# Performance work log

Measured on AMD Instinct MI355X. Metric: run time of the kernel, lower is better.

## Reference

```python
import jax, jax.numpy as jnp
import numpy as np

N = 50000
E = 400000
D = 128            # embedding_dim
NUM_RBF = 20
CUT_OFF = 5.0
SILU_SCALE = 1.0 / 0.6


def scaled_silu(x):
    return jax.nn.silu(x) * SILU_SCALE


def cosine_cutoff(x):
    return 0.5 * (1.0 + jnp.cos(x * jnp.pi / CUT_OFF)) * (x < CUT_OFF).astype(x.dtype)


def setup_inputs() -> dict:
    key = jax.random.key(0)
    ks = jax.random.split(key, 10)
    vectorial_feat = jax.random.normal(ks[0], (N, D, 3), dtype=jnp.float32)
    scalar_feat = jax.random.normal(ks[1], (N, D), dtype=jnp.float32)
    node_pos = jax.random.uniform(ks[2], (N, 3), dtype=jnp.float32) * 10.0
    source = jax.random.randint(ks[3], (E,), 0, N)
    offset = jax.random.randint(ks[4], (E,), 1, N)  # avoid self-loops -> no zero distance
    target = (source + offset) % N
    edge_index = jnp.stack([source, target], axis=0).astype(jnp.int64)
    # scalar_feat_proj: Linear(D,D) -> ScaledSiLU -> Linear(D, 3D)
    W1 = jax.random.normal(ks[5], (D, D), dtype=jnp.float32) * (1.0 / np.sqrt(D))
    b1 = jnp.zeros((D,), dtype=jnp.float32)
    W2 = jax.random.normal(ks[6], (D, 3 * D), dtype=jnp.float32) * (1.0 / np.sqrt(D))
    b2 = jnp.zeros((3 * D,), dtype=jnp.float32)
    # rbf_proj: Linear(NUM_RBF, 3D)
    Wr = jax.random.normal(ks[7], (NUM_RBF, 3 * D), dtype=jnp.float32) * (1.0 / np.sqrt(NUM_RBF))
    br = jnp.zeros((3 * D,), dtype=jnp.float32)
    return {"vectorial_feat": vectorial_feat, "scalar_feat": scalar_feat,
            "node_pos": node_pos, "edge_index": edge_index,
            "W1": W1, "b1": b1, "W2": W2, "b2": b2, "Wr": Wr, "br": br}


def reference(vectorial_feat, scalar_feat, node_pos, edge_index, W1, b1, W2, b2, Wr, br):
    freqs = jnp.arange(1, NUM_RBF + 1, dtype=jnp.float32) * jnp.pi  # [NUM_RBF]
    source, target = edge_index[0], edge_index[1]

    # node-level scalar projection: [N, 3D]
    s = scaled_silu(scalar_feat @ W1 + b1) @ W2 + b2

    # per-edge geometry
    rel = node_pos[target] - node_pos[source]                 # [E, 3]
    dist = jnp.sqrt(jnp.sum(rel * rel, axis=-1))              # [E]
    dist_scaled = dist / CUT_OFF
    rbf = jnp.sin(freqs[None, :] * dist_scaled[:, None]) / dist[:, None]  # [E, NUM_RBF]

    filt = cosine_cutoff(rbf @ Wr + br)                       # [E, 3D]

    message = (s[source] * filt).reshape(E, D, 3)             # [E, D, 3]
    scalar_msg = message[..., 0]                              # [E, D]
    equiv_msg = message[..., 1]                               # [E, D]
    invar_msg = message[..., 2]                               # [E, D]

    scalar_message = jax.ops.segment_sum(scalar_msg, target, num_segments=N)  # [N, D]

    direction = rel / dist[:, None]                           # [E, 3]
    vec_msg = (invar_msg[:, :, None] * direction[:, None, :]
               + equiv_msg[:, :, None] * vectorial_feat[source])  # [E, D, 3]
    vectorial_message = jax.ops.segment_sum(vec_msg, target, num_segments=N)  # [N, D, 3]

    return vectorial_message, scalar_message
```

## Files before the change

kernel.cpp:

```cpp
#include <hip/hip_runtime.h>
#include <hip/hip_fp16.h>
#include <math.h>
#include <stddef.h>

#define D_DIM 128
#define NUM_RBF 20
typedef unsigned short ushort_t;
typedef unsigned int uint_t;
typedef _Float16 h2v __attribute__((ext_vector_type(2)));
typedef _Float16 half8_t __attribute__((ext_vector_type(8)));
typedef float float4_t __attribute__((ext_vector_type(4)));
constexpr float PI_F = 3.14159265358979323846f;
constexpr float CUT_OFF_F = 5.0f;
constexpr float SILU_SCALE_F = 1.0f / 0.6f;

__device__ __forceinline__ uint_t pack2h(float a, float b) {
  __half2 h2 = __floats2half2_rn(a, b);
  return *reinterpret_cast<uint_t*>(&h2);
}
__device__ __forceinline__ float h2f(ushort_t u) {
  __half h = __ushort_as_half(u);
  return __half2float(h);
}
__device__ __forceinline__ h2v u2h2(uint_t u) {
  h2v r;
  __builtin_memcpy(&r, &u, 4);
  return r;
}

#if defined(__has_builtin)
#if __has_builtin(__builtin_amdgcn_fdot2)
#define HAVE_FDOT2 1
#endif
#endif

__device__ __forceinline__ float fdot2f(h2v a, h2v b, float c) {
#ifdef HAVE_FDOT2
  return __builtin_amdgcn_fdot2(a, b, c, false);
#else
  return c + (float)a.x * (float)b.x + (float)a.y * (float)b.y;
#endif
}

__device__ __forceinline__ void stage_wt(const float* __restrict__ W,
                                         _Float16* __restrict__ Wt, int t,
                                         int f4stride, int f4base) {
  const float4* Wv = reinterpret_cast<const float4*>(W);
#pragma unroll
  for (int i = 0; i < 8; ++i) {
    int pid = t + i * 256;
    int k = (pid >> 5) * 2;
    int nf = pid & 31;
    float4 a = Wv[(size_t)k * f4stride + f4base + nf];
    float4 b = Wv[(size_t)(k + 1) * f4stride + f4base + nf];
    const float av[4] = {a.x, a.y, a.z, a.w};
    const float bv[4] = {b.x, b.y, b.z, b.w};
    const int n0 = nf * 4;
#pragma unroll
    for (int j = 0; j < 4; ++j)
      *reinterpret_cast<uint_t*>(&Wt[(n0 + j) * 136 + k]) =
          pack2h(av[j], bv[j]);
  }
}

__global__ __launch_bounds__(256) void proj_kernel(
    const float* __restrict__ X, const float* __restrict__ W1,
    const float* __restrict__ b1, const float* __restrict__ W2,
    const float* __restrict__ b2, ushort_t* __restrict__ s_half, int N) {
  __shared__ alignas(16) _Float16 Xs[64 * 136];
  __shared__ alignas(16) _Float16 Wt[128 * 136];

  const int t = threadIdx.x;
  const int w = t >> 6;
  const int l = t & 63;
  const int nb = blockIdx.x * 64;

  {
    const float4* Xv = reinterpret_cast<const float4*>(X);
#pragma unroll
    for (int i = 0; i < 8; ++i) {
      int g = t + i * 256;
      int row = g >> 5, k0 = (g & 31) * 4;
      int node = nb + row;
      float4 v = (node < N) ? Xv[(size_t)nb * 32 + g]
                            : make_float4(0.f, 0.f, 0.f, 0.f);
      uint_t* dst = reinterpret_cast<uint_t*>(&Xs[row * 136 + k0]);
      dst[0] = pack2h(v.x, v.y);
      dst[1] = pack2h(v.z, v.w);
    }
  }
  stage_wt(W1, Wt, t, 32, 0);
  __syncthreads();

  const int arow = w * 16 + (l & 15);
  const int koff = (l >> 4) * 8;
  const int bcol = l & 15;

  half8_t af[4];
#pragma unroll
  for (int s = 0; s < 4; ++s)
    af[s] = *reinterpret_cast<const half8_t*>(&Xs[arow * 136 + s * 32 + koff]);

  float4_t acc[8];
#pragma unroll
  for (int c = 0; c < 8; ++c) {
    float4_t a = {0.f, 0.f, 0.f, 0.f};
#pragma unroll
    for (int s = 0; s < 4; ++s) {
      half8_t bf = *reinterpret_cast<const half8_t*>(
          &Wt[(c * 16 + bcol) * 136 + s * 32 + koff]);
      a = __builtin_amdgcn_mfma_f32_16x16x32_f16(af[s], bf, a, 0, 0, 0);
    }
    acc[c] = a;
  }

  __syncthreads();

#pragma unroll
  for (int c = 0; c < 8; ++c) {
    const int col = c * 16 + bcol;
    const float bv = b1[col];
#pragma unroll
    for (int r = 0; r < 4; ++r) {
      const int row = w * 16 + (l >> 4) * 4 + r;
      float hv = acc[c][r] + bv;
      hv = hv * SILU_SCALE_F / (1.0f + expf(-hv));
      Xs[row * 136 + col] = (_Float16)hv;
    }
  }
  stage_wt(W2, Wt, t, 96, 0);
  __syncthreads();

  half8_t ha[4];
#pragma unroll
  for (int s = 0; s < 4; ++s)
    ha[s] = *reinterpret_cast<const half8_t*>(&Xs[arow * 136 + s * 32 + koff]);

  for (int cn = 0; cn < 3; ++cn) {
    if (cn > 0) {
      __syncthreads();
      stage_wt(W2, Wt, t, 96, cn * 32);
      __syncthreads();
    }
#pragma unroll
    for (int c = 0; c < 8; ++c) {
      float4_t a = {0.f, 0.f, 0.f, 0.f};
#pragma unroll
      for (int s = 0; s < 4; ++s) {
        half8_t bf = *reinterpret_cast<const half8_t*>(
            &Wt[(c * 16 + bcol) * 136 + s * 32 + koff]);
        a = __builtin_amdgcn_mfma_f32_16x16x32_f16(ha[s], bf, a, 0, 0, 0);
      }
      const int gcol = cn * 128 + c * 16 + bcol;
      const float bv = b2[gcol];
#pragma unroll
      for (int r = 0; r < 4; ++r) {
        const int node = nb + w * 16 + (l >> 4) * 4 + r;
        if (node < N)
          s_half[(size_t)node * 384 + gcol] =
              __half_as_ushort(__float2half_rn(a[r] + bv));
      }
    }
  }
}

__global__ void vf_cast_kernel(const float* __restrict__ vf,
                               ushort_t* __restrict__ vf_half, int total8) {
  int i = blockIdx.x * 256 + threadIdx.x;
  if (i >= total8) return;
  const float4* v4 = reinterpret_cast<const float4*>(vf);
  float4 a = v4[2 * i], b = v4[2 * i + 1];
  uint4 r = make_uint4(pack2h(a.x, a.y), pack2h(a.z, a.w),
                       pack2h(b.x, b.y), pack2h(b.z, b.w));
  reinterpret_cast<uint4*>(vf_half)[i] = r;
}

__global__ void zero_kernel(int* __restrict__ p, int n) {
  int i = blockIdx.x * 256 + threadIdx.x;
  if (i < n) p[i] = 0;
}

__global__ void hist_kernel(const int* __restrict__ tgt, int* __restrict__ counts,
                            int E) {
  int e = blockIdx.x * 256 + threadIdx.x;
  if (e < E) atomicAdd(&counts[tgt[e]], 1);
}

__global__ void chunk_sum_kernel(const int* __restrict__ counts,
                                 int* __restrict__ chunk_sums, int N) {
  __shared__ int red[256];
  int b = blockIdx.x, t = threadIdx.x;
  int base = b * 1024 + t * 4;
  int s = 0;
#pragma unroll
  for (int j = 0; j < 4; ++j) s += (base + j < N) ? counts[base + j] : 0;
  red[t] = s;
  __syncthreads();
  for (int off = 128; off > 0; off >>= 1) {
    if (t < off) red[t] += red[t + off];
    __syncthreads();
  }
  if (t == 0) chunk_sums[b] = red[0];
}

__global__ void scan_chunks_kernel(int* __restrict__ chunk_sums,
                                   int* __restrict__ offsets, int nch, int N,
                                   int E) {
  int t = threadIdx.x;
  int v = (t < nch) ? chunk_sums[t] : 0;
  int orig = v;
#pragma unroll
  for (int off = 1; off < 64; off <<= 1) {
    int y = __shfl_up(v, off);
    if (t >= off) v += y;
  }
  if (t < nch) chunk_sums[t] = v - orig;
  if (t == 0) offsets[N] = E;
}

__global__ void scan_block_kernel(const int* __restrict__ counts,
                                  const int* __restrict__ chunk_off,
                                  int* __restrict__ offsets,
                                  int* __restrict__ cursor, int N) {
  __shared__ int part[256];
  int b = blockIdx.x, t = threadIdx.x;
  int base = b * 1024 + t * 4;
  int v[4];
#pragma unroll
  for (int j = 0; j < 4; ++j) v[j] = (base + j < N) ? counts[base + j] : 0;
  int local = v[0] + v[1] + v[2] + v[3];
  part[t] = local;
  __syncthreads();
  for (int off = 1; off < 256; off <<= 1) {
    int x = 0;
    if (t >= off) x = part[t - off];
    __syncthreads();
    if (t >= off) part[t] += x;
    __syncthreads();
  }
  int run = chunk_off[b] + (part[t] - local);
#pragma unroll
  for (int j = 0; j < 4; ++j) {
    if (base + j < N) {
      offsets[base + j] = run;
      cursor[base + j] = run;
      run += v[j];
    }
  }
}

__global__ void edge_geom_kernel(const float* __restrict__ pos,
                                 const int* __restrict__ src,
                                 const int* __restrict__ tgt,
                                 int* __restrict__ cursor,
                                 float4* __restrict__ dir4_s,
                                 uint_t* __restrict__ rbh_s,
                                 int* __restrict__ src_s, int E) {
  int e = blockIdx.x * 256 + threadIdx.x;
  if (e >= E) return;
  const int sn = src[e];
  const int tn = tgt[e];
  const float rx = pos[tn * 3 + 0] - pos[sn * 3 + 0];
  const float ry = pos[tn * 3 + 1] - pos[sn * 3 + 1];
  const float rz = pos[tn * 3 + 2] - pos[sn * 3 + 2];
  const float dist = sqrtf(rx * rx + ry * ry + rz * rz);
  const float inv = 1.0f / dist;

  const float ang = dist * (PI_F / CUT_OFF_F);
  float s1, c1;
  sincosf(ang, &s1, &c1);
  float sk = s1, ck = c1;
  float rb[NUM_RBF];
  rb[0] = s1 * inv;
#pragma unroll
  for (int r = 1; r < NUM_RBF; ++r) {
    float sn2 = sk * c1 + ck * s1;
    ck = ck * c1 - sk * s1;
    sk = sn2;
    rb[r] = sk * inv;
  }

  const int p = atomicAdd(&cursor[tn], 1);
  dir4_s[p] = make_float4(rx * inv, ry * inv, rz * inv, dist);
  src_s[p] = sn;
  uint_t us[10];
#pragma unroll
  for (int q = 0; q < 10; ++q) us[q] = pack2h(rb[2 * q], rb[2 * q + 1]);
  uint_t* o = rbh_s + (size_t)p * 12;
  *reinterpret_cast<uint4*>(o) = make_uint4(us[0], us[1], us[2], us[3]);
  *reinterpret_cast<uint4*>(o + 4) = make_uint4(us[4], us[5], us[6], us[7]);
  *reinterpret_cast<uint2*>(o + 8) = make_uint2(us[8], us[9]);
}

#define NODES_PER_BLOCK 16

__device__ __forceinline__ float cutoff_f(float x) {
  return (x < CUT_OFF_F) ? 0.5f * (1.0f + __cosf(x * (PI_F / CUT_OFF_F))) : 0.f;
}

struct EdgeData {
  float4 dir;
  uint_t rbu[10];
  float sx, sy, sz, vx, vy, vz;
};

__device__ __forceinline__ void load_edge(int idx, int sn, int d,
                                          const ushort_t* __restrict__ s_half,
                                          const ushort_t* __restrict__ vf_half,
                                          const float4* __restrict__ dir4_s,
                                          const uint_t* __restrict__ rbh_s,
                                          EdgeData& ed) {
  ed.dir = dir4_s[idx];
  const uint_t* o = rbh_s + (size_t)idx * 12;
  uint4 u0 = *reinterpret_cast<const uint4*>(o);
  uint4 u1 = *reinterpret_cast<const uint4*>(o + 4);
  uint2 u2 = *reinterpret_cast<const uint2*>(o + 8);
  ed.rbu[0] = u0.x; ed.rbu[1] = u0.y; ed.rbu[2] = u0.z; ed.rbu[3] = u0.w;
  ed.rbu[4] = u1.x; ed.rbu[5] = u1.y; ed.rbu[6] = u1.z; ed.rbu[7] = u1.w;
  ed.rbu[8] = u2.x; ed.rbu[9] = u2.y;
  const ushort_t* sr = s_half + (size_t)sn * 384 + 3 * d;
  ed.sx = h2f(sr[0]); ed.sy = h2f(sr[1]); ed.sz = h2f(sr[2]);
  const ushort_t* vr = vf_half + (size_t)sn * 384 + 3 * d;
  ed.vx = h2f(vr[0]); ed.vy = h2f(vr[1]); ed.vz = h2f(vr[2]);
}

__global__ __launch_bounds__(128) void node_kernel(
    const ushort_t* __restrict__ s_half, const ushort_t* __restrict__ vf_half,
    const float4* __restrict__ dir4_s, const uint_t* __restrict__ rbh_s,
    const int* __restrict__ src_s, const int* __restrict__ offsets,
    const float* __restrict__ Wr, const float* __restrict__ br,
    float* __restrict__ out, int N, int E) {
  const int d = threadIdx.x;
  const int lane = d & 63;

  h2v wr0h[10], wr1h[10], wr2h[10];
#pragma unroll
  for (int q = 0; q < 10; ++q) {
    h2v w;
    w.x = (_Float16)Wr[(2 * q) * 384 + 3 * d + 0];
    w.y = (_Float16)Wr[(2 * q + 1) * 384 + 3 * d + 0];
    wr0h[q] = w;
    w.x = (_Float16)Wr[(2 * q) * 384 + 3 * d + 1];
    w.y = (_Float16)Wr[(2 * q + 1) * 384 + 3 * d + 1];
    wr1h[q] = w;
    w.x = (_Float16)Wr[(2 * q) * 384 + 3 * d + 2];
    w.y = (_Float16)Wr[(2 * q + 1) * 384 + 3 * d + 2];
    wr2h[q] = w;
  }
  const float br0 = br[3 * d + 0];
  const float br1 = br[3 * d + 1];
  const float br2 = br[3 * d + 2];

  for (int nn = 0; nn < NODES_PER_BLOCK; ++nn) {
    const int n = blockIdx.x * NODES_PER_BLOCK + nn;
    if (n >= N) break;

    const int start = offsets[n];
    const int end = offsets[n + 1];

    float accs = 0.f, av0 = 0.f, av1 = 0.f, av2 = 0.f;

    for (int base = start; base < end; base += 64) {
      const int m = min(64, end - base);
      int ld = base + lane;
      if (ld >= E) ld = E - 1;
      const int sn_l = src_s[ld];

      int i = 0;
      for (; i + 2 <= m; i += 2) {
        const int sn0 = __shfl(sn_l, i);
        const int sn1 = __shfl(sn_l, i + 1);
        EdgeData e0, e1;
        load_edge(base + i, sn0, d, s_half, vf_half, dir4_s, rbh_s, e0);
        load_edge(base + i + 1, sn1, d, s_half, vf_half, dir4_s, rbh_s, e1);

#pragma unroll
        for (int u = 0; u < 2; ++u) {
          const EdgeData& ed = (u == 0) ? e0 : e1;
          float f0 = br0, f1 = br1, f2 = br2;
#pragma unroll
          for (int q = 0; q < 10; ++q) {
            h2v r = u2h2(ed.rbu[q]);
            f0 = fdot2f(r, wr0h[q], f0);
            f1 = fdot2f(r, wr1h[q], f1);
            f2 = fdot2f(r, wr2h[q], f2);
          }
          f0 = cutoff_f(f0);
          f1 = cutoff_f(f1);
          f2 = cutoff_f(f2);
          const float m0 = ed.sx * f0;
          const float m1 = ed.sy * f1;
          const float m2 = ed.sz * f2;
          accs += m0;
          av0 += m2 * ed.dir.x + m1 * ed.vx;
          av1 += m2 * ed.dir.y + m1 * ed.vy;
          av2 += m2 * ed.dir.z + m1 * ed.vz;
        }
      }
      if (i < m) {
        const int sn0 = __shfl(sn_l, i);
        EdgeData e0;
        load_edge(base + i, sn0, d, s_half, vf_half, dir4_s, rbh_s, e0);
        float f0 = br0, f1 = br1, f2 = br2;
#pragma unroll
        for (int q = 0; q < 10; ++q) {
          h2v r = u2h2(e0.rbu[q]);
          f0 = fdot2f(r, wr0h[q], f0);
          f1 = fdot2f(r, wr1h[q], f1);
          f2 = fdot2f(r, wr2h[q], f2);
        }
        f0 = cutoff_f(f0);
        f1 = cutoff_f(f1);
        f2 = cutoff_f(f2);
        const float m0 = e0.sx * f0;
        const float m1 = e0.sy * f1;
        const float m2 = e0.sz * f2;
        accs += m0;
        av0 += m2 * e0.dir.x + m1 * e0.vx;
        av1 += m2 * e0.dir.y + m1 * e0.vy;
        av2 += m2 * e0.dir.z + m1 * e0.vz;
      }
    }

    out[(size_t)n * 384 + 3 * d + 0] = av0;
    out[(size_t)n * 384 + 3 * d + 1] = av1;
    out[(size_t)n * 384 + 3 * d + 2] = av2;
    out[(size_t)N * 384 + (size_t)n * 128 + d] = accs;
  }
}

extern "C" void kernel_launch(void* const* d_in, const int* in_sizes, int n_in,
                              void* d_out, int out_size, void* d_ws,
                              size_t ws_size, hipStream_t stream) {
  const float* vf  = (const float*)d_in[0];
  const float* X   = (const float*)d_in[1];
  const float* pos = (const float*)d_in[2];
  const int* ei    = (const int*)d_in[3];
  const float* W1  = (const float*)d_in[4];
  const float* b1  = (const float*)d_in[5];
  const float* W2  = (const float*)d_in[6];
  const float* b2  = (const float*)d_in[7];
  const float* Wr  = (const float*)d_in[8];
  const float* br  = (const float*)d_in[9];

  const int N = in_sizes[1] / D_DIM;
  const int E = in_sizes[3] / 2;
  const int* srcI = ei;
  const int* tgtI = ei + E;
  float* out = (float*)d_out;

  char* w = (char*)d_ws;
  float4* dir4_s    = (float4*)w;   w += (size_t)E * sizeof(float4);
  uint_t* rbh_s     = (uint_t*)w;   w += (size_t)E * 12 * sizeof(uint_t);
  ushort_t* s_half  = (ushort_t*)w; w += (size_t)N * 384 * sizeof(ushort_t);
  ushort_t* vf_half = (ushort_t*)w; w += (size_t)N * 384 * sizeof(ushort_t);
  int* src_s        = (int*)w;      w += (size_t)E * sizeof(int);
  int* counts       = (int*)w;      w += (size_t)N * sizeof(int);
  int* offsets      = (int*)w;      w += (size_t)(N + 1) * sizeof(int);
  int* cursor       = (int*)w;      w += (size_t)N * sizeof(int);
  int* chunks       = (int*)w;      w += 64 * sizeof(int);

  const int nch = (N + 1023) / 1024;

  zero_kernel<<<(N + 255) / 256, 256, 0, stream>>>(counts, N);
  proj_kernel<<<(N + 63) / 64, 256, 0, stream>>>(X, W1, b1, W2, b2, s_half, N);
  vf_cast_kernel<<<(N * 384 / 8 + 255) / 256, 256, 0, stream>>>(vf, vf_half,
                                                                N * 384 / 8);
  hist_kernel<<<(E + 255) / 256, 256, 0, stream>>>(tgtI, counts, E);
  chunk_sum_kernel<<<nch, 256, 0, stream>>>(counts, chunks, N);
  scan_chunks_kernel<<<1, 64, 0, stream>>>(chunks, offsets, nch, N, E);
  scan_block_kernel<<<nch, 256, 0, stream>>>(counts, chunks, offsets, cursor, N);
  edge_geom_kernel<<<(E + 255) / 256, 256, 0, stream>>>(pos, srcI, tgtI, cursor,
                                                        dir4_s, rbh_s, src_s, E);
  node_kernel<<<(N + NODES_PER_BLOCK - 1) / NODES_PER_BLOCK, 128, 0, stream>>>(
      s_half, vf_half, dir4_s, rbh_s, src_s, offsets, Wr, br, out, N, E);
}
```

Measured before the change: 311.7 us.

## Fuse vf cast into projection kernel and interleave s and vf per channel

Result: no change. 307.1 us (-1.5%).

```diff
diff --git a/kernel.cpp b/kernel.cpp
--- a/kernel.cpp
+++ b/kernel.cpp
@@ -22,6 +22,8 @@
   __half h = __ushort_as_half(u);
   return __half2float(h);
 }
+__device__ __forceinline__ float h2f_lo(uint_t u) { return h2f((ushort_t)(u & 0xffffu)); }
+__device__ __forceinline__ float h2f_hi(uint_t u) { return h2f((ushort_t)(u >> 16)); }
 __device__ __forceinline__ h2v u2h2(uint_t u) {
   h2v r;
   __builtin_memcpy(&r, &u, 4);
@@ -66,9 +68,11 @@
 __global__ __launch_bounds__(256) void proj_kernel(
     const float* __restrict__ X, const float* __restrict__ W1,
     const float* __restrict__ b1, const float* __restrict__ W2,
-    const float* __restrict__ b2, ushort_t* __restrict__ s_half, int N) {
-  __shared__ alignas(16) _Float16 Xs[64 * 136];
-  __shared__ alignas(16) _Float16 Wt[128 * 136];
+    const float* __restrict__ b2, const float* __restrict__ vf,
+    uint_t* __restrict__ merged, int N) {
+  __shared__ alignas(16) _Float16 smem[26112];
+  _Float16* Xs = smem;
+  _Float16* Wt = smem + 8704;
 
   const int t = threadIdx.x;
   const int w = t >> 6;
@@ -136,6 +140,8 @@
   for (int s = 0; s < 4; ++s)
     ha[s] = *reinterpret_cast<const half8_t*>(&Xs[arow * 136 + s * 32 + koff]);
 
+  uint_t pk[3][8][2];
+#pragma unroll
   for (int cn = 0; cn < 3; ++cn) {
     if (cn > 0) {
       __syncthreads();
@@ -151,28 +157,45 @@
             &Wt[(c * 16 + bcol) * 136 + s * 32 + koff]);
         a = __builtin_amdgcn_mfma_f32_16x16x32_f16(ha[s], bf, a, 0, 0, 0);
       }
-      const int gcol = cn * 128 + c * 16 + bcol;
-      const float bv = b2[gcol];
-#pragma unroll
-      for (int r = 0; r < 4; ++r) {
-        const int node = nb + w * 16 + (l >> 4) * 4 + r;
-        if (node < N)
-          s_half[(size_t)node * 384 + gcol] =
-              __half_as_ushort(__float2half_rn(a[r] + bv));
+      const float bv = b2[cn * 128 + c * 16 + bcol];
+      pk[cn][c][0] = pack2h(a[0] + bv, a[1] + bv);
+      pk[cn][c][1] = pack2h(a[2] + bv, a[3] + bv);
+    }
+  }
+
+  __syncthreads();
+  ushort_t* sh = reinterpret_cast<ushort_t*>(smem);
+  {
+    const int rbase = w * 16 + (l >> 4) * 4;
+#pragma unroll
+    for (int cn = 0; cn < 3; ++cn)
+#pragma unroll
+      for (int c = 0; c < 8; ++c) {
+        const int gcol = cn * 128 + c * 16 + bcol;
+        sh[(rbase + 0) * 392 + gcol] = (ushort_t)(pk[cn][c][0] & 0xffffu);
+        sh[(rbase + 1) * 392 + gcol] = (ushort_t)(pk[cn][c][0] >> 16);
+        sh[(rbase + 2) * 392 + gcol] = (ushort_t)(pk[cn][c][1] & 0xffffu);
+        sh[(rbase + 3) * 392 + gcol] = (ushort_t)(pk[cn][c][1] >> 16);
       }
-    }
-  }
-}
-
-__global__ void vf_cast_kernel(const float* __restrict__ vf,
-                               ushort_t* __restrict__ vf_half, int total8) {
-  int i = blockIdx.x * 256 + threadIdx.x;
-  if (i >= total8) return;
-  const float4* v4 = reinterpret_cast<const float4*>(vf);
-  float4 a = v4[2 * i], b = v4[2 * i + 1];
-  uint4 r = make_uint4(pack2h(a.x, a.y), pack2h(a.z, a.w),
-                       pack2h(b.x, b.y), pack2h(b.z, b.w));
-  reinterpret_cast<uint4*>(vf_half)[i] = r;
+  }
+  __syncthreads();
+
+#pragma unroll 4
+  for (int k = 0; k < 32; ++k) {
+    const int P = k * 256 + t;
+    const int ln = P >> 7;
+    const int chan = P & 127;
+    const int node = nb + ln;
+    if (node < N) {
+      const ushort_t* sp = &sh[ln * 392 + 3 * chan];
+      const float* vp = vf + ((size_t)node * 128 + chan) * 3;
+      uint_t* mp = merged + ((size_t)node * 128 + chan) * 3;
+      mp[0] = (uint_t)sp[0] | ((uint_t)sp[1] << 16);
+      mp[1] = (uint_t)sp[2] |
+              ((uint_t)__half_as_ushort(__float2half_rn(vp[0])) << 16);
+      mp[2] = pack2h(vp[1], vp[2]);
+    }
+  }
 }
 
 __global__ void zero_kernel(int* __restrict__ p, int n) {
@@ -292,7 +315,7 @@
   *reinterpret_cast<uint2*>(o + 8) = make_uint2(us[8], us[9]);
 }
 
-#define NODES_PER_BLOCK 16
+#define NODES_PER_BLOCK 8
 
 __device__ __forceinline__ float cutoff_f(float x) {
   return (x < CUT_OFF_F) ? 0.5f * (1.0f + __cosf(x * (PI_F / CUT_OFF_F))) : 0.f;
@@ -301,12 +324,11 @@
 struct EdgeData {
   float4 dir;
   uint_t rbu[10];
-  float sx, sy, sz, vx, vy, vz;
+  uint_t su[3];
 };
 
 __device__ __forceinline__ void load_edge(int idx, int sn, int d,
-                                          const ushort_t* __restrict__ s_half,
-                                          const ushort_t* __restrict__ vf_half,
+                                          const uint_t* __restrict__ merged,
                                           const float4* __restrict__ dir4_s,
                                           const uint_t* __restrict__ rbh_s,
                                           EdgeData& ed) {
@@ -318,18 +340,15 @@
   ed.rbu[0] = u0.x; ed.rbu[1] = u0.y; ed.rbu[2] = u0.z; ed.rbu[3] = u0.w;
   ed.rbu[4] = u1.x; ed.rbu[5] = u1.y; ed.rbu[6] = u1.z; ed.rbu[7] = u1.w;
   ed.rbu[8] = u2.x; ed.rbu[9] = u2.y;
-  const ushort_t* sr = s_half + (size_t)sn * 384 + 3 * d;
-  ed.sx = h2f(sr[0]); ed.sy = h2f(sr[1]); ed.sz = h2f(sr[2]);
-  const ushort_t* vr = vf_half + (size_t)sn * 384 + 3 * d;
-  ed.vx = h2f(vr[0]); ed.vy = h2f(vr[1]); ed.vz = h2f(vr[2]);
+  const uint_t* mp = merged + ((size_t)sn * 128 + d) * 3;
+  ed.su[0] = mp[0]; ed.su[1] = mp[1]; ed.su[2] = mp[2];
 }
 
 __global__ __launch_bounds__(128) void node_kernel(
-    const ushort_t* __restrict__ s_half, const ushort_t* __restrict__ vf_half,
-    const float4* __restrict__ dir4_s, const uint_t* __restrict__ rbh_s,
-    const int* __restrict__ src_s, const int* __restrict__ offsets,
-    const float* __restrict__ Wr, const float* __restrict__ br,
-    float* __restrict__ out, int N, int E) {
+    const uint_t* __restrict__ merged, const float4* __restrict__ dir4_s,
+    const uint_t* __restrict__ rbh_s, const int* __restrict__ src_s,
+    const int* __restrict__ offsets, const float* __restrict__ Wr,
+    const float* __restrict__ br, float* __restrict__ out, int N, int E) {
   const int d = threadIdx.x;
   const int lane = d & 63;
 
@@ -371,8 +390,8 @@
         const int sn0 = __shfl(sn_l, i);
         const int sn1 = __shfl(sn_l, i + 1);
         EdgeData e0, e1;
-        load_edge(base + i, sn0, d, s_half, vf_half, dir4_s, rbh_s, e0);
-        load_edge(base + i + 1, sn1, d, s_half, vf_half, dir4_s, rbh_s, e1);
+        load_edge(base + i, sn0, d, merged, dir4_s, rbh_s, e0);
+        load_edge(base + i + 1, sn1, d, merged, dir4_s, rbh_s, e1);
 
 #pragma unroll
         for (int u = 0; u < 2; ++u) {
@@ -388,19 +407,19 @@
           f0 = cutoff_f(f0);
           f1 = cutoff_f(f1);
           f2 = cutoff_f(f2);
-          const float m0 = ed.sx * f0;
-          const float m1 = ed.sy * f1;
-          const float m2 = ed.sz * f2;
+          const float m0 = h2f_lo(ed.su[0]) * f0;
+          const float m1 = h2f_hi(ed.su[0]) * f1;
+          const float m2 = h2f_lo(ed.su[1]) * f2;
           accs += m0;
-          av0 += m2 * ed.dir.x + m1 * ed.vx;
-          av1 += m2 * ed.dir.y + m1 * ed.vy;
-          av2 += m2 * ed.dir.z + m1 * ed.vz;
+          av0 += m2 * ed.dir.x + m1 * h2f_hi(ed.su[1]);
+          av1 += m2 * ed.dir.y + m1 * h2f_lo(ed.su[2]);
+          av2 += m2 * ed.dir.z + m1 * h2f_hi(ed.su[2]);
         }
       }
       if (i < m) {
         const int sn0 = __shfl(sn_l, i);
         EdgeData e0;
-        load_edge(base + i, sn0, d, s_half, vf_half, dir4_s, rbh_s, e0);
+        load_edge(base + i, sn0, d, merged, dir4_s, rbh_s, e0);
         float f0 = br0, f1 = br1, f2 = br2;
 #pragma unroll
         for (int q = 0; q < 10; ++q) {
@@ -412,13 +431,13 @@
         f0 = cutoff_f(f0);
         f1 = cutoff_f(f1);
         f2 = cutoff_f(f2);
-        const float m0 = e0.sx * f0;
-        const float m1 = e0.sy * f1;
-        const float m2 = e0.sz * f2;
+        const float m0 = h2f_lo(e0.su[0]) * f0;
+        const float m1 = h2f_hi(e0.su[0]) * f1;
+        const float m2 = h2f_lo(e0.su[1]) * f2;
         accs += m0;
-        av0 += m2 * e0.dir.x + m1 * e0.vx;
-        av1 += m2 * e0.dir.y + m1 * e0.vy;
-        av2 += m2 * e0.dir.z + m1 * e0.vz;
+        av0 += m2 * e0.dir.x + m1 * h2f_hi(e0.su[1]);
+        av1 += m2 * e0.dir.y + m1 * h2f_lo(e0.su[2]);
+        av2 += m2 * e0.dir.z + m1 * h2f_hi(e0.su[2]);
       }
     }
 
@@ -450,22 +469,20 @@
   float* out = (float*)d_out;
 
   char* w = (char*)d_ws;
-  float4* dir4_s    = (float4*)w;   w += (size_t)E * sizeof(float4);
-  uint_t* rbh_s     = (uint_t*)w;   w += (size_t)E * 12 * sizeof(uint_t);
-  ushort_t* s_half  = (ushort_t*)w; w += (size_t)N * 384 * sizeof(ushort_t);
-  ushort_t* vf_half = (ushort_t*)w; w += (size_t)N * 384 * sizeof(ushort_t);
-  int* src_s        = (int*)w;      w += (size_t)E * sizeof(int);
-  int* counts       = (int*)w;      w += (size_t)N * sizeof(int);
-  int* offsets      = (int*)w;      w += (size_t)(N + 1) * sizeof(int);
-  int* cursor       = (int*)w;      w += (size_t)N * sizeof(int);
-  int* chunks       = (int*)w;      w += 64 * sizeof(int);
+  float4* dir4_s = (float4*)w;  w += (size_t)E * sizeof(float4);
+  uint_t* rbh_s  = (uint_t*)w;  w += (size_t)E * 12 * sizeof(uint_t);
+  uint_t* merged = (uint_t*)w;  w += (size_t)N * 128 * 3 * sizeof(uint_t);
+  int* src_s     = (int*)w;     w += (size_t)E * sizeof(int);
+  int* counts    = (int*)w;     w += (size_t)N * sizeof(int);
+  int* offsets   = (int*)w;     w += (size_t)(N + 1) * sizeof(int);
+  int* cursor    = (int*)w;     w += (size_t)N * sizeof(int);
+  int* chunks    = (int*)w;     w += 64 * sizeof(int);
 
   const int nch = (N + 1023) / 1024;
 
   zero_kernel<<<(N + 255) / 256, 256, 0, stream>>>(counts, N);
-  proj_kernel<<<(N + 63) / 64, 256, 0, stream>>>(X, W1, b1, W2, b2, s_half, N);
-  vf_cast_kernel<<<(N * 384 / 8 + 255) / 256, 256, 0, stream>>>(vf, vf_half,
-                                                                N * 384 / 8);
+  proj_kernel<<<(N + 63) / 64, 256, 0, stream>>>(X, W1, b1, W2, b2, vf, merged,
+                                                 N);
   hist_kernel<<<(E + 255) / 256, 256, 0, stream>>>(tgtI, counts, E);
   chunk_sum_kernel<<<nch, 256, 0, stream>>>(counts, chunks, N);
   scan_chunks_kernel<<<1, 64, 0, stream>>>(chunks, offsets, nch, N, E);
@@ -473,5 +490,5 @@
   edge_geom_kernel<<<(E + 255) / 256, 256, 0, stream>>>(pos, srcI, tgtI, cursor,
                                                         dir4_s, rbh_s, src_s, E);
   node_kernel<<<(N + NODES_PER_BLOCK - 1) / NODES_PER_BLOCK, 128, 0, stream>>>(
-      s_half, vf_half, dir4_s, rbh_s, src_s, offsets, Wr, br, out, N, E);
-}
+      merged, dir4_s, rbh_s, src_s, offsets, Wr, br, out, N, E);
+}
```
